# Optimization experiments

Hardware: AMD Instinct MI355X
Metric: run time of the kernel (lower is better)

Reference implementation:

```python
import jax, jax.numpy as jnp
import numpy as np

N_NODES = 50000
N_EDGES = 1000000
IN_C = 128
HID_C = 128
N_REL = 8


def rgcn_conv(x, W, root, b, src, dst, et, n_rel):
    # PyG-style RGCNConv: per-relation linear transform of source features,
    # mean-aggregated per (target node, relation), plus root transform + bias.
    n = x.shape[0]
    h = jnp.einsum('nd,rdh->nrh', x, W)          # [N, R, H] per-relation transforms
    msgs = h[src, et]                            # [E, H] gather per-edge message
    seg = dst * n_rel + et                       # combined (node, relation) segment id
    agg = jax.ops.segment_sum(msgs, seg, num_segments=n * n_rel)        # [N*R, H]
    cnt = jax.ops.segment_sum(jnp.ones_like(msgs[:, 0]), seg, num_segments=n * n_rel)
    agg = agg / jnp.maximum(cnt, 1.0)[:, None]   # mean over edges of each relation
    return agg.reshape(n, n_rel, -1).sum(axis=1) + x @ root + b


def setup_inputs() -> dict:
    key = jax.random.key(0)
    ks = jax.random.split(key, 12)
    s = 1.0 / np.sqrt(IN_C)
    sh = 1.0 / np.sqrt(HID_C)
    return {
        'x': jax.random.normal(ks[0], (N_NODES, IN_C), dtype=jnp.float32),
        'ei': jax.random.randint(ks[1], (2, N_EDGES), 0, N_NODES, dtype=jnp.int32),
        'et': jax.random.randint(ks[2], (N_EDGES,), 0, N_REL, dtype=jnp.int32),
        'W1': jax.random.normal(ks[3], (N_REL, IN_C, HID_C), dtype=jnp.float32) * s,
        'root1': jax.random.normal(ks[4], (IN_C, HID_C), dtype=jnp.float32) * s,
        'b1': jnp.zeros((HID_C,), dtype=jnp.float32),
        'W2': jax.random.normal(ks[5], (N_REL, HID_C, HID_C), dtype=jnp.float32) * sh,
        'root2': jax.random.normal(ks[6], (HID_C, HID_C), dtype=jnp.float32) * sh,
        'b2': jnp.zeros((HID_C,), dtype=jnp.float32),
        'lin_W': jax.random.normal(ks[7], (HID_C, HID_C), dtype=jnp.float32) * sh,
        'lin_b': jnp.zeros((HID_C,), dtype=jnp.float32),
    }


def reference(x, ei, et, W1, root1, b1, W2, root2, b2, lin_W, lin_b):
    src, dst = ei[0], ei[1]
    h = jax.nn.relu(rgcn_conv(x, W1, root1, b1, src, dst, et, N_REL))
    h = rgcn_conv(h, W2, root2, b2, src, dst, et, N_REL)
    return h @ lin_W + lin_b
```

## Files before the change

kernel.cpp:

```cpp
#include <hip/hip_runtime.h>
#include <hip/hip_bf16.h>

#define N_NODES 50000
#define N_EDGES 1000000
#define C       128
#define N_REL   8
#define N_SEG   (N_NODES * N_REL)
#define KTOT    (N_REL * C + C)
#define KC_CNT  (KTOT / 32)
#define A_STRIDE 1160
#define NCHUNK  ((N_SEG + 1023) / 1024)
#define MV_N    (N_SEG + 1 + N_EDGES)
#define NBLK    (N_NODES / 16)
#define FE_BLK  ((N_EDGES + 511) / 512)

typedef __hip_bfloat16  bf16;
typedef __hip_bfloat162 bf162;
typedef __attribute__((ext_vector_type(8))) short short8;
typedef __attribute__((ext_vector_type(4))) float f32x4;

__device__ __forceinline__ size_t frag_index(int k, int n) {
    int nt = n >> 4, n15 = n & 15;
    int kc = k >> 5, quad = (k >> 3) & 3, j = k & 7;
    int lane = quad * 16 + n15;
    return ((size_t)(nt * KC_CNT + kc) * 64 + lane) * 8 + j;
}

#define CVT_BLOCKS ((N_NODES * C / 2) / 256)
#define CNT_BLOCKS ((N_EDGES + 255) / 256)
__global__ void prep_kernel(const float2* __restrict__ xf, unsigned int* __restrict__ xb,
                            const int* __restrict__ dst, const int* __restrict__ et,
                            int* __restrict__ cnt) {
    int bid = blockIdx.x;
    if (bid < CVT_BLOCKS) {
        int i = bid * 256 + threadIdx.x;
        float2 v = xf[i];
        union { bf162 h; unsigned int u; } cv;
        cv.h = bf162(__float2bfloat16(v.x), __float2bfloat16(v.y));
        xb[i] = cv.u;
    } else {
        int e = (bid - CVT_BLOCKS) * 256 + threadIdx.x;
        if (e < N_EDGES) atomicAdd(&cnt[dst[e] * N_REL + et[e]], 1);
    }
}

#define RP_B (KTOT * C / 256)
__global__ void scanA_kernel(const int* __restrict__ cnt, int* __restrict__ offs,
                             int* __restrict__ partials,
                             const float* __restrict__ W1, const float* __restrict__ root1,
                             const float* __restrict__ W2, const float* __restrict__ root2,
                             const float* __restrict__ linW,
                             const float* __restrict__ b2, const float* __restrict__ linb,
                             bf16* __restrict__ Bp1, bf16* __restrict__ Bp2,
                             float* __restrict__ b2p) {
    int bid = blockIdx.x;
    int t   = threadIdx.x;
    if (bid < NCHUNK) {
        __shared__ int tot[256];
        int base = bid * 1024 + t * 4;
        int v0 = (base + 0 < N_SEG) ? cnt[base + 0] : 0;
        int v1 = (base + 1 < N_SEG) ? cnt[base + 1] : 0;
        int v2 = (base + 2 < N_SEG) ? cnt[base + 2] : 0;
        int v3 = (base + 3 < N_SEG) ? cnt[base + 3] : 0;
        int tsum = v0 + v1 + v2 + v3;
        tot[t] = tsum;
        __syncthreads();
        for (int d = 1; d < 256; d <<= 1) {
            int x = tot[t];
            int y = (t >= d) ? tot[t - d] : 0;
            __syncthreads();
            tot[t] = x + y;
            __syncthreads();
        }
        int excl = tot[t] - tsum;
        if (base + 0 < N_SEG) offs[base + 0] = excl;
        if (base + 1 < N_SEG) offs[base + 1] = excl + v0;
        if (base + 2 < N_SEG) offs[base + 2] = excl + v0 + v1;
        if (base + 3 < N_SEG) offs[base + 3] = excl + v0 + v1 + v2;
        if (t == 255) partials[bid] = tot[255];
    } else if (bid < NCHUNK + RP_B) {
        int idx = (bid - NCHUNK) * 256 + t;
        int k = idx >> 7, n = idx & 127;
        float val;
        if (k < N_REL * C) val = W1[(size_t)k * C + n];
        else               val = root1[(size_t)(k - N_REL * C) * C + n];
        Bp1[frag_index(k, n)] = __float2bfloat16(val);
    } else if (bid < NCHUNK + 2 * RP_B) {
        int idx = (bid - NCHUNK - RP_B) * 256 + t;
        int k = idx >> 7, n = idx & 127;
        const float* row = (k < N_REL * C) ? (W2 + (size_t)k * C)
                                           : (root2 + (size_t)(k - N_REL * C) * C);
        float acc = 0.f;
        for (int m = 0; m < C; m++)
            acc += row[m] * linW[(size_t)m * C + n];
        Bp2[frag_index(k, n)] = __float2bfloat16(acc);
    } else {
        if (t < 128) {
            float acc = linb[t];
            for (int m = 0; m < C; m++)
                acc += b2[m] * linW[(size_t)m * C + t];
            b2p[t] = acc;
        }
    }
}

__global__ void fillB_kernel(const int* __restrict__ src, const int* __restrict__ dst,
                             const int* __restrict__ et,
                             const int* __restrict__ offs_raw,
                             const int* __restrict__ partials,
                             int* __restrict__ offs_final,
                             int* __restrict__ ticket,
                             int* __restrict__ srcs_out) {
    __shared__ int s[512];
    int t = threadIdx.x;
    int bid = blockIdx.x;
    s[t] = (t < NCHUNK) ? partials[t] : 0;
    __syncthreads();
    for (int d = 1; d < 512; d <<= 1) {
        int x = s[t];
        int y = (t >= d) ? s[t - d] : 0;
        __syncthreads();
        s[t] = x + y;
        __syncthreads();
    }
    if (bid < NCHUNK) {
        int add = (bid == 0) ? 0 : s[bid - 1];
        int base = bid * 1024 + t * 2;
#pragma unroll
        for (int j = 0; j < 2; j++) {
            int idx = base + j;
            if (idx < N_SEG) offs_final[idx] = offs_raw[idx] + add;
        }
        if (bid == 0 && t == 0) offs_final[N_SEG] = N_EDGES;
    } else {
        int e = (bid - NCHUNK) * 512 + t;
        if (e < N_EDGES) {
            int seg = dst[e] * N_REL + et[e];
            int chunk = seg >> 10;
            int base = offs_raw[seg] + ((chunk == 0) ? 0 : s[chunk - 1]);
            int pos = base + atomicAdd(&ticket[seg], 1);
            srcs_out[pos] = src[e];
        }
    }
}

template <int RELU, int OUT_F32, int COPY_CSR>
__global__ __launch_bounds__(512, 6) void fused_layer(
        const unsigned int* __restrict__ featu,
        const int*   __restrict__ offs,
        const int*   __restrict__ srcs,
        const short8* __restrict__ Bp,
        const float* __restrict__ bias,
        void* __restrict__ outp,
        int* __restrict__ offs2, int* __restrict__ srcs2)
{
    __shared__ __align__(16) unsigned int At[16 * (A_STRIDE / 2)];
    __shared__ int offsL[129];
    const int tid  = threadIdx.x;
    const int lane = tid & 63;
    const int w    = tid >> 6;
    const int v0   = blockIdx.x * 16;

    if (tid < 129) offsL[tid] = offs[v0 * 8 + tid];
    if (tid < 64)  At[(tid >> 2) * (A_STRIDE / 2) + 576 + (tid & 3)] = 0u;

    if (COPY_CSR) {
        for (int i = blockIdx.x * 512 + tid; i < MV_N; i += NBLK * 512) {
            if (i < N_SEG + 1) offs2[i] = offs[i];
            else               srcs2[i - (N_SEG + 1)] = srcs[i - (N_SEG + 1)];
        }
    }

    for (int q = tid; q < 16 * 64; q += 512) {
        int node = q >> 6, pch = q & 63;
        At[node * (A_STRIDE / 2) + 512 + pch] = featu[(size_t)(v0 + node) * 64 + pch];
    }
    __syncthreads();

    {
        const int segLo = w * 16;
        const int segHi = segLo + 16;
        int curSeg = segLo;
        int segEnd = offsL[curSeg + 1];
        int i      = offsL[segLo];
        const int eend = offsL[segHi];
        float a0 = 0.f, a1 = 0.f;

        while (i + 16 <= eend) {
            const int ib = __builtin_amdgcn_readfirstlane(i);
            int sv[16];
#pragma unroll
            for (int j = 0; j < 16; j++) sv[j] = srcs[ib + j];
            unsigned int vals[16];
#pragma unroll
            for (int j = 0; j < 16; j++) vals[j] = featu[(size_t)sv[j] * 64 + lane];
#pragma unroll
            for (int j = 0; j < 16; j++) {
                while (i + j == segEnd) {
                    int b = offsL[curSeg];
                    float inv = (segEnd > b) ? 1.0f / (float)(segEnd - b) : 0.0f;
                    union { bf162 h; unsigned int u; } cv;
                    cv.h = bf162(__float2bfloat16(a0 * inv), __float2bfloat16(a1 * inv));
                    At[(curSeg >> 3) * (A_STRIDE / 2) + (curSeg & 7) * 64 + lane] = cv.u;
                    a0 = 0.f; a1 = 0.f;
                    curSeg++;
                    segEnd = offsL[curSeg + 1];
                }
                union { bf162 h; unsigned int u; } uv; uv.u = vals[j];
                a0 += __low2float(uv.h);
                a1 += __high2float(uv.h);
            }
            i += 16;
        }
        {
            int m = eend - i;
            const int ib = __builtin_amdgcn_readfirstlane(i);
            int sv[16];
#pragma unroll
            for (int j = 0; j < 16; j++) if (j < m) sv[j] = srcs[ib + j];
            unsigned int vals[16];
#pragma unroll
            for (int j = 0; j < 16; j++) if (j < m) vals[j] = featu[(size_t)sv[j] * 64 + lane];
#pragma unroll
            for (int j = 0; j < 16; j++) {
                if (j < m) {
                    while (i + j == segEnd) {
                        int b = offsL[curSeg];
                        float inv = (segEnd > b) ? 1.0f / (float)(segEnd - b) : 0.0f;
                        union { bf162 h; unsigned int u; } cv;
                        cv.h = bf162(__float2bfloat16(a0 * inv), __float2bfloat16(a1 * inv));
                        At[(curSeg >> 3) * (A_STRIDE / 2) + (curSeg & 7) * 64 + lane] = cv.u;
                        a0 = 0.f; a1 = 0.f;
                        curSeg++;
                        segEnd = offsL[curSeg + 1];
                    }
                    union { bf162 h; unsigned int u; } uv; uv.u = vals[j];
                    a0 += __low2float(uv.h);
                    a1 += __high2float(uv.h);
                }
            }
        }
        while (curSeg < segHi) {
            int b = offsL[curSeg], e2 = offsL[curSeg + 1];
            float inv = (e2 > b) ? 1.0f / (float)(e2 - b) : 0.0f;
            union { bf162 h; unsigned int u; } cv;
            cv.h = bf162(__float2bfloat16(a0 * inv), __float2bfloat16(a1 * inv));
            At[(curSeg >> 3) * (A_STRIDE / 2) + (curSeg & 7) * 64 + lane] = cv.u;
            a0 = 0.f; a1 = 0.f;
            curSeg++;
        }
    }
    __syncthreads();

    const int quad = lane >> 4, n15 = lane & 15;
    f32x4 acc = {0.f, 0.f, 0.f, 0.f};
    const short* Ash = (const short*)At;

    short8 b0 = Bp[(size_t)(w * KC_CNT) * 64 + lane];
#pragma unroll 4
    for (int kc = 0; kc < KC_CNT; kc++) {
        short8 cb0 = b0;
        if (kc + 1 < KC_CNT)
            b0 = Bp[(size_t)(w * KC_CNT + kc + 1) * 64 + lane];
        short8 a = *reinterpret_cast<const short8*>(Ash + n15 * A_STRIDE + kc * 32 + quad * 8);
        acc = __builtin_amdgcn_mfma_f32_16x16x32_bf16(a, cb0, acc, 0, 0, 0);
    }

    {
        int col = w * 16 + n15;
        float bv = bias[col];
#pragma unroll
        for (int r = 0; r < 4; r++) {
            int m = quad * 4 + r;
            float v = acc[r] + bv;
            if (RELU) v = fmaxf(v, 0.f);
            if (OUT_F32) ((float*)outp)[(size_t)(v0 + m) * C + col] = v;
            else         ((bf16*)outp)[(size_t)(v0 + m) * C + col] = __float2bfloat16(v);
        }
    }
}

extern "C" void kernel_launch(void* const* d_in, const int* in_sizes, int n_in,
                              void* d_out, int out_size, void* d_ws, size_t ws_size,
                              hipStream_t stream) {
    const float* x     = (const float*)d_in[0];
    const int*   ei    = (const int*)d_in[1];
    const int*   et    = (const int*)d_in[2];
    const float* W1    = (const float*)d_in[3];
    const float* root1 = (const float*)d_in[4];
    const float* b1    = (const float*)d_in[5];
    const float* W2    = (const float*)d_in[6];
    const float* root2 = (const float*)d_in[7];
    const float* b2    = (const float*)d_in[8];
    const float* linW  = (const float*)d_in[9];
    const float* linb  = (const float*)d_in[10];
    const int* src = ei;
    const int* dst = ei + N_EDGES;

    char* ob = (char*)d_out;
    int* cnt_i    = (int*)(ob + 0);
    int* ticket   = (int*)(ob + 1600000);
    int* offs_t   = (int*)(ob + 3200000);
    int* partials = (int*)(ob + 4800256);
    int* offs_f   = (int*)(ob + 4803072);
    int* srcs_t   = (int*)(ob + 6403328);
    unsigned int* xb16 = (unsigned int*)(ob + 10500000);

    char* eb = (char*)d_in[1];
    int* offs2 = (int*)(eb + 0);
    int* srcs2 = (int*)(eb + 1600256);

    char* xbuf = (char*)d_in[0];
    unsigned int* h1 = (unsigned int*)xbuf;
    bf16*  Bp1 = (bf16*)(xbuf + 13000000);
    bf16*  Bp2 = (bf16*)(xbuf + 13295104);
    float* b2p = (float*)(xbuf + 13590016);

    float* out = (float*)d_out;

    hipMemsetAsync(cnt_i, 0, 3200000, stream);
    prep_kernel<<<CVT_BLOCKS + CNT_BLOCKS, 256, 0, stream>>>(
        (const float2*)x, xb16, dst, et, cnt_i);
    scanA_kernel<<<NCHUNK + 2 * RP_B + 1, 256, 0, stream>>>(
        cnt_i, offs_t, partials, W1, root1, W2, root2, linW, b2, linb,
        Bp1, Bp2, b2p);
    fillB_kernel<<<NCHUNK + FE_BLK, 512, 0, stream>>>(
        src, dst, et, offs_t, partials, offs_f, ticket, srcs_t);

    fused_layer<1, 0, 1><<<NBLK, 512, 0, stream>>>(
        xb16, offs_f, srcs_t, (const short8*)Bp1, b1, (void*)h1, offs2, srcs2);
    fused_layer<0, 1, 0><<<NBLK, 512, 0, stream>>>(
        h1, offs2, srcs2, (const short8*)Bp2, b2p, (void*)out, nullptr, nullptr);

    (void)in_sizes; (void)n_in; (void)out_size; (void)d_ws; (void)ws_size;
}
```

Measured before the change: 332.8 us.

## Software-pipeline edge gathers and tile the W2·linW weight fold in shared memory

Result: no change. 327.1 us (-1.7%).

```diff
diff --git a/kernel.cpp b/kernel.cpp
--- a/kernel.cpp
+++ b/kernel.cpp
@@ -44,7 +44,8 @@
     }
 }
 
-#define RP_B (KTOT * C / 256)
+#define RP_B  (KTOT * C / 256)
+#define RPT_B ((KTOT / 16) * (C / 16))
 __global__ void scanA_kernel(const int* __restrict__ cnt, int* __restrict__ offs,
                              int* __restrict__ partials,
                              const float* __restrict__ W1, const float* __restrict__ root1,
@@ -85,15 +86,32 @@
         if (k < N_REL * C) val = W1[(size_t)k * C + n];
         else               val = root1[(size_t)(k - N_REL * C) * C + n];
         Bp1[frag_index(k, n)] = __float2bfloat16(val);
-    } else if (bid < NCHUNK + 2 * RP_B) {
-        int idx = (bid - NCHUNK - RP_B) * 256 + t;
-        int k = idx >> 7, n = idx & 127;
-        const float* row = (k < N_REL * C) ? (W2 + (size_t)k * C)
-                                           : (root2 + (size_t)(k - N_REL * C) * C);
+    } else if (bid < NCHUNK + RP_B + RPT_B) {
+        __shared__ float Wt[16][128];
+        __shared__ float Lt[128][16];
+        int tileid = bid - NCHUNK - RP_B;
+        int kt = tileid >> 3;
+        int n0 = (tileid & 7) * 16;
+        int k0 = kt * 16;
+        const float* baseW = (k0 < N_REL * C) ? (W2 + (size_t)k0 * C)
+                                              : (root2 + (size_t)(k0 - N_REL * C) * C);
+#pragma unroll
+        for (int r = 0; r < 8; r++) {
+            int idx = t + r * 256;
+            Wt[idx >> 7][idx & 127] = baseW[idx];
+        }
+#pragma unroll
+        for (int r = 0; r < 8; r++) {
+            int idx = t + r * 256;
+            Lt[idx >> 4][idx & 15] = linW[(size_t)(idx >> 4) * C + n0 + (idx & 15)];
+        }
+        __syncthreads();
+        int ty = t >> 4, tx = t & 15;
         float acc = 0.f;
-        for (int m = 0; m < C; m++)
-            acc += row[m] * linW[(size_t)m * C + n];
-        Bp2[frag_index(k, n)] = __float2bfloat16(acc);
+#pragma unroll 8
+        for (int m = 0; m < 128; m++)
+            acc += Wt[ty][m] * Lt[m][tx];
+        Bp2[frag_index(k0 + ty, n0 + tx)] = __float2bfloat16(acc);
     } else {
         if (t < 128) {
             float acc = linb[t];
@@ -186,14 +204,28 @@
         const int eend = offsL[segHi];
         float a0 = 0.f, a1 = 0.f;
 
-        while (i + 16 <= eend) {
+        unsigned int vals[16];
+        bool have = (i + 16 <= eend);
+        if (have) {
             const int ib = __builtin_amdgcn_readfirstlane(i);
             int sv[16];
 #pragma unroll
             for (int j = 0; j < 16; j++) sv[j] = srcs[ib + j];
-            unsigned int vals[16];
 #pragma unroll
             for (int j = 0; j < 16; j++) vals[j] = featu[(size_t)sv[j] * 64 + lane];
+        }
+        while (have) {
+            const int inext = i + 16;
+            const bool havenext = (inext + 16 <= eend);
+            unsigned int vals2[16];
+            if (havenext) {
+                const int ib2 = __builtin_amdgcn_readfirstlane(inext);
+                int sv2[16];
+#pragma unroll
+                for (int j = 0; j < 16; j++) sv2[j] = srcs[ib2 + j];
+#pragma unroll
+                for (int j = 0; j < 16; j++) vals2[j] = featu[(size_t)sv2[j] * 64 + lane];
+            }
 #pragma unroll
             for (int j = 0; j < 16; j++) {
                 while (i + j == segEnd) {
@@ -210,7 +242,12 @@
                 a0 += __low2float(uv.h);
                 a1 += __high2float(uv.h);
             }
-            i += 16;
+            i = inext;
+            have = havenext;
+            if (havenext) {
+#pragma unroll
+                for (int j = 0; j < 16; j++) vals[j] = vals2[j];
+            }
         }
         {
             int m = eend - i;
@@ -218,9 +255,9 @@
             int sv[16];
 #pragma unroll
             for (int j = 0; j < 16; j++) if (j < m) sv[j] = srcs[ib + j];
-            unsigned int vals[16];
-#pragma unroll
-            for (int j = 0; j < 16; j++) if (j < m) vals[j] = featu[(size_t)sv[j] * 64 + lane];
+            unsigned int tvals[16];
+#pragma unroll
+            for (int j = 0; j < 16; j++) if (j < m) tvals[j] = featu[(size_t)sv[j] * 64 + lane];
 #pragma unroll
             for (int j = 0; j < 16; j++) {
                 if (j < m) {
@@ -234,7 +271,7 @@
                         curSeg++;
                         segEnd = offsL[curSeg + 1];
                     }
-                    union { bf162 h; unsigned int u; } uv; uv.u = vals[j];
+                    union { bf162 h; unsigned int u; } uv; uv.u = tvals[j];
                     a0 += __low2float(uv.h);
                     a1 += __high2float(uv.h);
                 }
@@ -304,7 +341,7 @@
     int* partials = (int*)(ob + 4800256);
     int* offs_f   = (int*)(ob + 4803072);
     int* srcs_t   = (int*)(ob + 6403328);
-    unsigned int* xb16 = (unsigned int*)(ob + 10500000);
+    unsigned int* xb16 = (unsigned int*)(ob + 10485760);
 
     char* eb = (char*)d_in[1];
     int* offs2 = (int*)(eb + 0);
@@ -312,16 +349,16 @@
 
     char* xbuf = (char*)d_in[0];
     unsigned int* h1 = (unsigned int*)xbuf;
-    bf16*  Bp1 = (bf16*)(xbuf + 13000000);
-    bf16*  Bp2 = (bf16*)(xbuf + 13295104);
-    float* b2p = (float*)(xbuf + 13590016);
+    bf16*  Bp1 = (bf16*)(xbuf + 13000192);
+    bf16*  Bp2 = (bf16*)(xbuf + 13295360);
+    float* b2p = (float*)(xbuf + 13590528);
 
     float* out = (float*)d_out;
 
     hipMemsetAsync(cnt_i, 0, 3200000, stream);
     prep_kernel<<<CVT_BLOCKS + CNT_BLOCKS, 256, 0, stream>>>(
         (const float2*)x, xb16, dst, et, cnt_i);
-    scanA_kernel<<<NCHUNK + 2 * RP_B + 1, 256, 0, stream>>>(
+    scanA_kernel<<<NCHUNK + RP_B + RPT_B + 1, 256, 0, stream>>>(
         cnt_i, offs_t, partials, W1, root1, W2, root2, linW, b2, linb,
         Bp1, Bp2, b2p);
     fillB_kernel<<<NCHUNK + FE_BLK, 512, 0, stream>>>(
```
